# Performance work log

Measured on AMD Instinct MI355X. Metric: run time of the kernel, lower is better.

Reference implementation:

```python
import jax, jax.numpy as jnp
import numpy as np

B, ES, HS, NL, NOUT, T = 16384, 64, 64, 3, 2, 128


def setup_inputs() -> dict:
    key = jax.random.key(0)
    ks = jax.random.split(key, 9)
    k = 1.0 / np.sqrt(HS)
    u = lambda kk, shape: jax.random.uniform(kk, shape, jnp.float32, -k, k)
    return {
        "agentFutureTrajEnc": jax.random.normal(ks[0], (B, ES), jnp.float32),
        "emb_w": u(ks[1], (ES, ES)),
        "emb_b": u(ks[2], (ES,)),
        "w_ih": u(ks[3], (NL, 3 * HS, ES)),
        "w_hh": u(ks[4], (NL, 3 * HS, HS)),
        "b_ih": u(ks[5], (NL, 3 * HS)),
        "b_hh": u(ks[6], (NL, 3 * HS)),
        "out_w": u(ks[7], (NOUT, HS)),
        "out_b": u(ks[8], (NOUT,)),
        "target_length": T,
        "batch_size": B,
    }


def _gru_cell(x, h, Wi, Wh, bi, bh):
    # PyTorch GRU cell math: gates ordered (r, z, n)
    gi = x @ Wi.T + bi            # (B, 3*hs)
    gh = h @ Wh.T + bh            # (B, 3*hs)
    ir, iz, inn = jnp.split(gi, 3, axis=-1)
    hr, hz, hn = jnp.split(gh, 3, axis=-1)
    r = jax.nn.sigmoid(ir + hr)
    z = jax.nn.sigmoid(iz + hz)
    n = jnp.tanh(inn + r * hn)
    return (1.0 - z) * n + z * h


def reference(agentFutureTrajEnc, emb_w, emb_b, w_ih, w_hh, b_ih, b_hh, out_w, out_b,
              target_length, batch_size):
    nl = w_ih.shape[0]
    # hidden initialized by repeating the encoding across layers: (nl, B, hs)
    h0 = jnp.broadcast_to(agentFutureTrajEnc[None], (nl,) + agentFutureTrajEnc.shape)

    def step(carry, _):
        x, h = carry                      # x: (B, es), h: (nl, B, hs)
        inp = x @ emb_w.T + emb_b         # embedding Linear(es->es)
        new_h = []
        for l in range(nl):               # small fixed layer loop
            hl = _gru_cell(inp, h[l], w_ih[l], w_hh[l], b_ih[l], b_hh[l])
            new_h.append(hl)
            inp = hl
        h = jnp.stack(new_h)              # (nl, B, hs)
        out = inp @ out_w.T + out_b       # (B, nout)
        return (h[-1], h), out            # next input is top-layer hidden

    _, outs = jax.lax.scan(step, (agentFutureTrajEnc, h0), None, length=target_length)
    return jnp.transpose(outs, (1, 0, 2))  # (B, T, nout)
```

## Files before the change

### kernel.cpp

```cpp
#include <hip/hip_runtime.h>


#define ESZ   64
#define HSZ   64
#define TLEN  128
#define NOUTC 2
#define NT    2
#define LDW   72
#define TB32  (32*LDW)
#define L2E   1.44269504f

typedef _Float16 half8 __attribute__((ext_vector_type(8)));
typedef _Float16 half4 __attribute__((ext_vector_type(4)));
typedef float    floatx4 __attribute__((ext_vector_type(4)));
typedef float    floatx2 __attribute__((ext_vector_type(2)));

#define MFMA(a, b, c) __builtin_amdgcn_mfma_f32_16x16x32_f16((a), (b), (c), 0, 0, 0)

__global__ __launch_bounds__(768, 3) void gru_pipe(
    const float* __restrict__ enc,
    const float* __restrict__ emb_w,
    const float* __restrict__ emb_b,
    const float* __restrict__ w_ih,
    const float* __restrict__ w_hh,
    const float* __restrict__ b_ih,
    const float* __restrict__ b_hh,
    const float* __restrict__ out_w,
    const float* __restrict__ out_b,
    float* __restrict__ out)
{
    __shared__ _Float16 s_hl[3 * NT * 2 * TB32];
    __shared__ float    s_btmp[3 * 64];
    __shared__ int      s_flag[3 * NT];

    const int tid  = threadIdx.x;
    const int wave = tid >> 6, lane = tid & 63;
    const int l = wave >> 2, g = wave & 3;
    const int q = lane >> 4, c = lane & 15;
    const int u  = (g << 4) | c;
    const int u4 = (g << 4) | (q << 2);
    const long wgbase = (long)blockIdx.x * 64;

    if (tid < 512) {
        const int row = tid >> 3, k0 = (tid & 7) << 3;
        const int j = row >> 5, rr = row & 31;
        const float* p = enc + (wgbase + row) * ESZ + k0;
        floatx4 s0 = *(const floatx4*)p;
        floatx4 s1 = *(const floatx4*)(p + 4);
        half8 v;
        #pragma unroll
        for (int x = 0; x < 4; ++x) { v[x] = (_Float16)s0[x]; v[4 + x] = (_Float16)s1[x]; }
        #pragma unroll
        for (int ly = 0; ly < 3; ++ly)
            *(half8*)&s_hl[((ly * NT + j) * 2 + 1) * TB32 + rr * LDW + k0] = v;
    }
    if (tid < 3 * NT) s_flag[tid] = 0;

    auto ldw8s = [&](const float* p, float sc) {
        floatx4 a = *(const floatx4*)p, b = *(const floatx4*)(p + 4);
        half8 v;
        #pragma unroll
        for (int x = 0; x < 4; ++x) { v[x] = (_Float16)(a[x] * sc); v[4 + x] = (_Float16)(b[x] * sc); }
        return v;
    };
    half8 fR[4], fZ[4], fNi[2], fNh[2], fO[2];
    fO[0] = fO[1] = half8{};
    if (l == 0) {
        const float* wi = w_ih;
        const float* wh = w_hh;
        floatx4 aR[4], aZ[4], aN[4];
        #pragma unroll
        for (int x = 0; x < 4; ++x) { aR[x] = {0,0,0,0}; aZ[x] = {0,0,0,0}; aN[x] = {0,0,0,0}; }
        float bR = 0.f, bZ = 0.f, bN = 0.f;
        for (int k4 = 0; k4 < 64; k4 += 4) {
            floatx4 wr4 = *(const floatx4*)(wi + (u) * 64 + k4);
            floatx4 wz4 = *(const floatx4*)(wi + (64 + u) * 64 + k4);
            floatx4 wn4 = *(const floatx4*)(wi + (128 + u) * 64 + k4);
            floatx4 be4 = *(const floatx4*)(emb_b + k4);
            #pragma unroll
            for (int kk = 0; kk < 4; ++kk) {
                const float* er = emb_w + (k4 + kk) * 64;
                floatx4 e0 = *(const floatx4*)(er + q * 8);
                floatx4 e1 = *(const floatx4*)(er + q * 8 + 4);
                floatx4 e2 = *(const floatx4*)(er + 32 + q * 8);
                floatx4 e3 = *(const floatx4*)(er + 32 + q * 8 + 4);
                const float wr = wr4[kk], wz = wz4[kk], wn = wn4[kk];
                aR[0] += wr * e0; aR[1] += wr * e1; aR[2] += wr * e2; aR[3] += wr * e3;
                aZ[0] += wz * e0; aZ[1] += wz * e1; aZ[2] += wz * e2; aZ[3] += wz * e3;
                aN[0] += wn * e0; aN[1] += wn * e1; aN[2] += wn * e2; aN[3] += wn * e3;
                bR += wr * be4[kk]; bZ += wz * be4[kk]; bN += wn * be4[kk];
            }
        }
        #pragma unroll
        for (int x = 0; x < 4; ++x) {
            fR[0][x] = (_Float16)(-L2E * aR[0][x]);   fR[0][4 + x] = (_Float16)(-L2E * aR[1][x]);
            fR[1][x] = (_Float16)(-L2E * aR[2][x]);   fR[1][4 + x] = (_Float16)(-L2E * aR[3][x]);
            fZ[0][x] = (_Float16)(-L2E * aZ[0][x]);   fZ[0][4 + x] = (_Float16)(-L2E * aZ[1][x]);
            fZ[1][x] = (_Float16)(-L2E * aZ[2][x]);   fZ[1][4 + x] = (_Float16)(-L2E * aZ[3][x]);
            fNi[0][x] = (_Float16)(2*L2E * aN[0][x]); fNi[0][4 + x] = (_Float16)(2*L2E * aN[1][x]);
            fNi[1][x] = (_Float16)(2*L2E * aN[2][x]); fNi[1][4 + x] = (_Float16)(2*L2E * aN[3][x]);
        }
        fR[2]  = ldw8s(wh + (u) * 64 + q * 8, -L2E);        fR[3]  = ldw8s(wh + (u) * 64 + 32 + q * 8, -L2E);
        fZ[2]  = ldw8s(wh + (64 + u) * 64 + q * 8, -L2E);   fZ[3]  = ldw8s(wh + (64 + u) * 64 + 32 + q * 8, -L2E);
        fNh[0] = ldw8s(wh + (128 + u) * 64 + q * 8, 2*L2E); fNh[1] = ldw8s(wh + (128 + u) * 64 + 32 + q * 8, 2*L2E);
        if (q == 0) {
            s_btmp[u] = bR; s_btmp[64 + u] = bZ; s_btmp[128 + u] = bN;
        }
        const int oc = (c < NOUTC) ? c : 0;
        fO[0] = ldw8s(out_w + oc * 64 + q * 8, 1.f);
        fO[1] = ldw8s(out_w + oc * 64 + 32 + q * 8, 1.f);
    } else {
        const float* wi = w_ih + l * 3 * HSZ * ESZ;
        const float* wh = w_hh + l * 3 * HSZ * ESZ;
        fR[0]  = ldw8s(wi + (u) * 64 + q * 8, -L2E);        fR[1]  = ldw8s(wi + (u) * 64 + 32 + q * 8, -L2E);
        fR[2]  = ldw8s(wh + (u) * 64 + q * 8, -L2E);        fR[3]  = ldw8s(wh + (u) * 64 + 32 + q * 8, -L2E);
        fZ[0]  = ldw8s(wi + (64 + u) * 64 + q * 8, -L2E);   fZ[1]  = ldw8s(wi + (64 + u) * 64 + 32 + q * 8, -L2E);
        fZ[2]  = ldw8s(wh + (64 + u) * 64 + q * 8, -L2E);   fZ[3]  = ldw8s(wh + (64 + u) * 64 + 32 + q * 8, -L2E);
        fNi[0] = ldw8s(wi + (128 + u) * 64 + q * 8, 2*L2E); fNi[1] = ldw8s(wi + (128 + u) * 64 + 32 + q * 8, 2*L2E);
        fNh[0] = ldw8s(wh + (128 + u) * 64 + q * 8, 2*L2E); fNh[1] = ldw8s(wh + (128 + u) * 64 + 32 + q * 8, 2*L2E);
    }
    __syncthreads();

    floatx4 bR4, bZ4, bNi4, bNh4;
    if (l == 0) {
        #pragma unroll
        for (int i = 0; i < 4; ++i) {
            bR4[i]  = -L2E * (s_btmp[u4 + i] + b_ih[u4 + i] + b_hh[u4 + i]);
            bZ4[i]  = -L2E * (s_btmp[64 + u4 + i] + b_ih[64 + u4 + i] + b_hh[64 + u4 + i]);
            bNi4[i] = 2.f * L2E * (s_btmp[128 + u4 + i] + b_ih[128 + u4 + i]);
            bNh4[i] = 2.f * L2E * b_hh[128 + u4 + i];
        }
    } else {
        const int b0 = l * 192;
        floatx4 bi0 = *(const floatx4*)(b_ih + b0 + u4),       bh0 = *(const floatx4*)(b_hh + b0 + u4);
        floatx4 bi1 = *(const floatx4*)(b_ih + b0 + 64 + u4),  bh1 = *(const floatx4*)(b_hh + b0 + 64 + u4);
        floatx4 bi2 = *(const floatx4*)(b_ih + b0 + 128 + u4), bh2 = *(const floatx4*)(b_hh + b0 + 128 + u4);
        #pragma unroll
        for (int i = 0; i < 4; ++i) {
            bR4[i]  = -L2E * (bi0[i] + bh0[i]);
            bZ4[i]  = -L2E * (bi1[i] + bh1[i]);
            bNi4[i] = 2.f * L2E * bi2[i];
            bNh4[i] = 2.f * L2E * bh2[i];
        }
    }
    const float ob0 = out_b[0], ob1 = out_b[1];

    floatx4 ca00 = *(const floatx4*)(enc + (wgbase +  0 + c) * 64 + u4);
    floatx4 ca01 = *(const floatx4*)(enc + (wgbase + 16 + c) * 64 + u4);
    floatx4 ca10 = *(const floatx4*)(enc + (wgbase + 32 + c) * 64 + u4);
    floatx4 ca11 = *(const floatx4*)(enc + (wgbase + 48 + c) * 64 + u4);

    const int ar = c * LDW + (q << 3);
    const int fh = l * NT, fx = ((l == 0) ? 2 : (l - 1)) * NT;
    const int myj = g >> 1, mys = g & 1;

    auto iter = [&](const int j, floatx4& cs0, floatx4& cs1, const int t,
                    const int parh, const int parw) {
        { volatile const int* f = &s_flag[fh + j]; const int tg = 4 * t; while (*f < tg) {} }
        asm volatile("" ::: "memory");
        const _Float16* hb = s_hl + ((fh + j) * 2 + parh) * TB32;
        half8 ah00 = *(const half8*)(hb + ar),             ah01 = *(const half8*)(hb + ar + 32);
        half8 ah10 = *(const half8*)(hb + ar + 16 * LDW),  ah11 = *(const half8*)(hb + ar + 16 * LDW + 32);
        floatx4 accr0 = bR4, accz0 = bZ4, accnh0 = bNh4;
        floatx4 accr1 = bR4, accz1 = bZ4, accnh1 = bNh4;
        accr0  = MFMA(fR[2], ah00, accr0);   accr0  = MFMA(fR[3], ah01, accr0);
        accz0  = MFMA(fZ[2], ah00, accz0);   accz0  = MFMA(fZ[3], ah01, accz0);
        accnh0 = MFMA(fNh[0], ah00, accnh0); accnh0 = MFMA(fNh[1], ah01, accnh0);
        accr1  = MFMA(fR[2], ah10, accr1);   accr1  = MFMA(fR[3], ah11, accr1);
        accz1  = MFMA(fZ[2], ah10, accz1);   accz1  = MFMA(fZ[3], ah11, accz1);
        accnh1 = MFMA(fNh[0], ah10, accnh1); accnh1 = MFMA(fNh[1], ah11, accnh1);
        { volatile const int* f = &s_flag[fx + j]; const int tg = (l == 0) ? 4 * t : 4 * t + 4; while (*f < tg) {} }
        asm volatile("" ::: "memory");
        const _Float16* xb = (l == 0) ? s_hl + ((2 * NT + j) * 2 + parh) * TB32
                                      : s_hl + (((l - 1) * NT + j) * 2 + parw) * TB32;
        half8 bx00 = *(const half8*)(xb + ar),             bx01 = *(const half8*)(xb + ar + 32);
        half8 bx10 = *(const half8*)(xb + ar + 16 * LDW),  bx11 = *(const half8*)(xb + ar + 16 * LDW + 32);
        accr0  = MFMA(fR[0], bx00, accr0);   accr0  = MFMA(fR[1], bx01, accr0);
        accz0  = MFMA(fZ[0], bx00, accz0);   accz0  = MFMA(fZ[1], bx01, accz0);
        floatx4 accni0 = bNi4;
        accni0 = MFMA(fNi[0], bx00, accni0); accni0 = MFMA(fNi[1], bx01, accni0);
        accr1  = MFMA(fR[0], bx10, accr1);   accr1  = MFMA(fR[1], bx11, accr1);
        accz1  = MFMA(fZ[0], bx10, accz1);   accz1  = MFMA(fZ[1], bx11, accz1);
        floatx4 accni1 = bNi4;
        accni1 = MFMA(fNi[0], bx10, accni1); accni1 = MFMA(fNi[1], bx11, accni1);
        _Float16* hw = s_hl + ((fh + j) * 2 + parw) * TB32 + c * LDW + u4;
        {
            half4 hv4; floatx4 hnew;
            #pragma unroll
            for (int i = 0; i < 4; ++i) {
                const float r  = __builtin_amdgcn_rcpf(1.f + __builtin_amdgcn_exp2f(accr0[i]));
                const float z  = __builtin_amdgcn_rcpf(1.f + __builtin_amdgcn_exp2f(accz0[i]));
                const float a  = accni0[i] + r * accnh0[i];
                const float n  = 1.f - 2.f * __builtin_amdgcn_rcpf(1.f + __builtin_amdgcn_exp2f(a));
                const float hv = n + z * (cs0[i] - n);
                hnew[i] = hv; hv4[i] = (_Float16)hv;
            }
            *(half4*)hw = hv4;
            cs0 = hnew;
        }
        {
            half4 hv4; floatx4 hnew;
            #pragma unroll
            for (int i = 0; i < 4; ++i) {
                const float r  = __builtin_amdgcn_rcpf(1.f + __builtin_amdgcn_exp2f(accr1[i]));
                const float z  = __builtin_amdgcn_rcpf(1.f + __builtin_amdgcn_exp2f(accz1[i]));
                const float a  = accni1[i] + r * accnh1[i];
                const float n  = 1.f - 2.f * __builtin_amdgcn_rcpf(1.f + __builtin_amdgcn_exp2f(a));
                const float hv = n + z * (cs1[i] - n);
                hnew[i] = hv; hv4[i] = (_Float16)hv;
            }
            *(half4*)(hw + 16 * LDW) = hv4;
            cs1 = hnew;
        }
        asm volatile("s_waitcnt lgkmcnt(0)" ::: "memory");
        if (lane == 0) atomicAdd(&s_flag[fh + j], 1);
        if (l == 0 && myj == j && t >= 1) {
            const half8 ox0 = mys ? bx10 : bx00;
            const half8 ox1 = mys ? bx11 : bx01;
            floatx4 oa = {ob0, ob1, 0.f, 0.f};
            oa = MFMA(fO[0], ox0, oa);
            oa = MFMA(fO[1], ox1, oa);
            if (q == 0) {
                const long row = wgbase + j * 32 + mys * 16 + c;
                *(floatx2*)(out + (row * TLEN + (t - 1)) * NOUTC) = floatx2{oa[0], oa[1]};
            }
        }
    };

    for (int tt = 0; tt < TLEN; tt += 2) {
        iter(0, ca00, ca01, tt,     1, 0);
        iter(1, ca10, ca11, tt,     1, 0);
        iter(0, ca00, ca01, tt + 1, 0, 1);
        iter(1, ca10, ca11, tt + 1, 0, 1);
    }

    if (l == 0) {
        const int j = myj;
        { volatile const int* f = &s_flag[2 * NT + j]; while (*f < 4 * TLEN) {} }
        asm volatile("" ::: "memory");
        const _Float16* xb = s_hl + ((2 * NT + j) * 2 + 1) * TB32 + mys * 16 * LDW;
        half8 bx0 = *(const half8*)(xb + ar), bx1 = *(const half8*)(xb + ar + 32);
        floatx4 oa = {ob0, ob1, 0.f, 0.f};
        oa = MFMA(fO[0], bx0, oa);
        oa = MFMA(fO[1], bx1, oa);
        if (q == 0) {
            const long row = wgbase + j * 32 + mys * 16 + c;
            *(floatx2*)(out + (row * TLEN + 127) * NOUTC) = floatx2{oa[0], oa[1]};
        }
    }
}

extern "C" void kernel_launch(void* const* d_in, const int* in_sizes, int n_in,
                              void* d_out, int out_size, void* d_ws, size_t ws_size,
                              hipStream_t stream) {
    (void)in_sizes; (void)n_in; (void)d_ws; (void)ws_size; (void)out_size;
    const int grid = 16384 / 64;
    gru_pipe<<<grid, 768, 0, stream>>>(
        (const float*)d_in[0],
        (const float*)d_in[1],
        (const float*)d_in[2],
        (const float*)d_in[3],
        (const float*)d_in[4],
        (const float*)d_in[5],
        (const float*)d_in[6],
        (const float*)d_in[7],
        (const float*)d_in[8],
        (float*)d_out);
}
```

Before: 450.3 us.

## Replace spin-flag layer pipeline with barrier-scheduled wavefront over four row tiles

Drops the per-tile LDS flag counters and busy-wait spinning between the three layer wave groups. Splits the 64-row block into four 16-row tiles and runs a fixed staggered schedule where each layer group handles one tile per phase, with __syncthreads between phases. This removes spin polling and atomics, and each visit now works on a single 16-row tile, so MFMA work per visit is halved. In exchange it adds four block-wide barriers per step, and the tight wavefront may leave some groups idle.

```diff
diff --git a/kernel.cpp b/kernel.cpp
--- a/kernel.cpp
+++ b/kernel.cpp
@@ -5,9 +5,8 @@
 #define HSZ   64
 #define TLEN  128
 #define NOUTC 2
-#define NT    2
 #define LDW   72
-#define TB32  (32*LDW)
+#define TB16  (16*LDW)
 #define L2E   1.44269504f
 
 typedef _Float16 half8 __attribute__((ext_vector_type(8)));
@@ -29,9 +28,8 @@
     const float* __restrict__ out_b,
     float* __restrict__ out)
 {
-    __shared__ _Float16 s_hl[3 * NT * 2 * TB32];
+    __shared__ _Float16 s_hl[3 * 4 * 2 * TB16];
     __shared__ float    s_btmp[3 * 64];
-    __shared__ int      s_flag[3 * NT];
 
     const int tid  = threadIdx.x;
     const int wave = tid >> 6, lane = tid & 63;
@@ -43,7 +41,7 @@
 
     if (tid < 512) {
         const int row = tid >> 3, k0 = (tid & 7) << 3;
-        const int j = row >> 5, rr = row & 31;
+        const int j = row >> 4, rr = row & 15;
         const float* p = enc + (wgbase + row) * ESZ + k0;
         floatx4 s0 = *(const floatx4*)p;
         floatx4 s1 = *(const floatx4*)(p + 4);
@@ -52,9 +50,8 @@
         for (int x = 0; x < 4; ++x) { v[x] = (_Float16)s0[x]; v[4 + x] = (_Float16)s1[x]; }
         #pragma unroll
         for (int ly = 0; ly < 3; ++ly)
-            *(half8*)&s_hl[((ly * NT + j) * 2 + 1) * TB32 + rr * LDW + k0] = v;
-    }
-    if (tid < 3 * NT) s_flag[tid] = 0;
+            *(half8*)&s_hl[((ly * 4 + j) * 2 + 1) * TB16 + rr * LDW + k0] = v;
+    }
 
     auto ldw8s = [&](const float* p, float sc) {
         floatx4 a = *(const floatx4*)p, b = *(const floatx4*)(p + 4);
@@ -145,106 +142,81 @@
     }
     const float ob0 = out_b[0], ob1 = out_b[1];
 
-    floatx4 ca00 = *(const floatx4*)(enc + (wgbase +  0 + c) * 64 + u4);
-    floatx4 ca01 = *(const floatx4*)(enc + (wgbase + 16 + c) * 64 + u4);
-    floatx4 ca10 = *(const floatx4*)(enc + (wgbase + 32 + c) * 64 + u4);
-    floatx4 ca11 = *(const floatx4*)(enc + (wgbase + 48 + c) * 64 + u4);
+    floatx4 ca0 = *(const floatx4*)(enc + (wgbase +  0 + c) * 64 + u4);
+    floatx4 ca1 = *(const floatx4*)(enc + (wgbase + 16 + c) * 64 + u4);
+    floatx4 ca2 = *(const floatx4*)(enc + (wgbase + 32 + c) * 64 + u4);
+    floatx4 ca3 = *(const floatx4*)(enc + (wgbase + 48 + c) * 64 + u4);
 
     const int ar = c * LDW + (q << 3);
-    const int fh = l * NT, fx = ((l == 0) ? 2 : (l - 1)) * NT;
-    const int myj = g >> 1, mys = g & 1;
-
-    auto iter = [&](const int j, floatx4& cs0, floatx4& cs1, const int t,
-                    const int parh, const int parw) {
-        { volatile const int* f = &s_flag[fh + j]; const int tg = 4 * t; while (*f < tg) {} }
-        asm volatile("" ::: "memory");
-        const _Float16* hb = s_hl + ((fh + j) * 2 + parh) * TB32;
-        half8 ah00 = *(const half8*)(hb + ar),             ah01 = *(const half8*)(hb + ar + 32);
-        half8 ah10 = *(const half8*)(hb + ar + 16 * LDW),  ah11 = *(const half8*)(hb + ar + 16 * LDW + 32);
-        floatx4 accr0 = bR4, accz0 = bZ4, accnh0 = bNh4;
-        floatx4 accr1 = bR4, accz1 = bZ4, accnh1 = bNh4;
-        accr0  = MFMA(fR[2], ah00, accr0);   accr0  = MFMA(fR[3], ah01, accr0);
-        accz0  = MFMA(fZ[2], ah00, accz0);   accz0  = MFMA(fZ[3], ah01, accz0);
-        accnh0 = MFMA(fNh[0], ah00, accnh0); accnh0 = MFMA(fNh[1], ah01, accnh0);
-        accr1  = MFMA(fR[2], ah10, accr1);   accr1  = MFMA(fR[3], ah11, accr1);
-        accz1  = MFMA(fZ[2], ah10, accz1);   accz1  = MFMA(fZ[3], ah11, accz1);
-        accnh1 = MFMA(fNh[0], ah10, accnh1); accnh1 = MFMA(fNh[1], ah11, accnh1);
-        { volatile const int* f = &s_flag[fx + j]; const int tg = (l == 0) ? 4 * t : 4 * t + 4; while (*f < tg) {} }
-        asm volatile("" ::: "memory");
-        const _Float16* xb = (l == 0) ? s_hl + ((2 * NT + j) * 2 + parh) * TB32
-                                      : s_hl + (((l - 1) * NT + j) * 2 + parw) * TB32;
-        half8 bx00 = *(const half8*)(xb + ar),             bx01 = *(const half8*)(xb + ar + 32);
-        half8 bx10 = *(const half8*)(xb + ar + 16 * LDW),  bx11 = *(const half8*)(xb + ar + 16 * LDW + 32);
-        accr0  = MFMA(fR[0], bx00, accr0);   accr0  = MFMA(fR[1], bx01, accr0);
-        accz0  = MFMA(fZ[0], bx00, accz0);   accz0  = MFMA(fZ[1], bx01, accz0);
-        floatx4 accni0 = bNi4;
-        accni0 = MFMA(fNi[0], bx00, accni0); accni0 = MFMA(fNi[1], bx01, accni0);
-        accr1  = MFMA(fR[0], bx10, accr1);   accr1  = MFMA(fR[1], bx11, accr1);
-        accz1  = MFMA(fZ[0], bx10, accz1);   accz1  = MFMA(fZ[1], bx11, accz1);
-        floatx4 accni1 = bNi4;
-        accni1 = MFMA(fNi[0], bx10, accni1); accni1 = MFMA(fNi[1], bx11, accni1);
-        _Float16* hw = s_hl + ((fh + j) * 2 + parw) * TB32 + c * LDW + u4;
-        {
-            half4 hv4; floatx4 hnew;
-            #pragma unroll
-            for (int i = 0; i < 4; ++i) {
-                const float r  = __builtin_amdgcn_rcpf(1.f + __builtin_amdgcn_exp2f(accr0[i]));
-                const float z  = __builtin_amdgcn_rcpf(1.f + __builtin_amdgcn_exp2f(accz0[i]));
-                const float a  = accni0[i] + r * accnh0[i];
-                const float n  = 1.f - 2.f * __builtin_amdgcn_rcpf(1.f + __builtin_amdgcn_exp2f(a));
-                const float hv = n + z * (cs0[i] - n);
-                hnew[i] = hv; hv4[i] = (_Float16)hv;
-            }
-            *(half4*)hw = hv4;
-            cs0 = hnew;
-        }
-        {
-            half4 hv4; floatx4 hnew;
-            #pragma unroll
-            for (int i = 0; i < 4; ++i) {
-                const float r  = __builtin_amdgcn_rcpf(1.f + __builtin_amdgcn_exp2f(accr1[i]));
-                const float z  = __builtin_amdgcn_rcpf(1.f + __builtin_amdgcn_exp2f(accz1[i]));
-                const float a  = accni1[i] + r * accnh1[i];
-                const float n  = 1.f - 2.f * __builtin_amdgcn_rcpf(1.f + __builtin_amdgcn_exp2f(a));
-                const float hv = n + z * (cs1[i] - n);
-                hnew[i] = hv; hv4[i] = (_Float16)hv;
-            }
-            *(half4*)(hw + 16 * LDW) = hv4;
-            cs1 = hnew;
-        }
-        asm volatile("s_waitcnt lgkmcnt(0)" ::: "memory");
-        if (lane == 0) atomicAdd(&s_flag[fh + j], 1);
-        if (l == 0 && myj == j && t >= 1) {
-            const half8 ox0 = mys ? bx10 : bx00;
-            const half8 ox1 = mys ? bx11 : bx01;
+
+    auto visit = [&](const int ll, const int j, floatx4& cs, const int t) {
+        const int parw = t & 1;
+        const _Float16* hb = s_hl + ((ll * 4 + j) * 2 + (parw ^ 1)) * TB16;
+        half8 ah0 = *(const half8*)(hb + ar);
+        half8 ah1 = *(const half8*)(hb + ar + 32);
+        floatx4 accr = bR4, accz = bZ4, accnh = bNh4;
+        accr  = MFMA(fR[2], ah0, accr);   accr  = MFMA(fR[3], ah1, accr);
+        accz  = MFMA(fZ[2], ah0, accz);   accz  = MFMA(fZ[3], ah1, accz);
+        accnh = MFMA(fNh[0], ah0, accnh); accnh = MFMA(fNh[1], ah1, accnh);
+        const _Float16* xb = (ll == 0) ? s_hl + ((8 + j) * 2 + (parw ^ 1)) * TB16
+                                       : s_hl + (((ll - 1) * 4 + j) * 2 + parw) * TB16;
+        half8 bx0 = *(const half8*)(xb + ar);
+        half8 bx1 = *(const half8*)(xb + ar + 32);
+        accr = MFMA(fR[0], bx0, accr); accr = MFMA(fR[1], bx1, accr);
+        accz = MFMA(fZ[0], bx0, accz); accz = MFMA(fZ[1], bx1, accz);
+        floatx4 accni = bNi4;
+        accni = MFMA(fNi[0], bx0, accni); accni = MFMA(fNi[1], bx1, accni);
+        _Float16* hw = s_hl + ((ll * 4 + j) * 2 + parw) * TB16 + c * LDW + u4;
+        half4 hv4; floatx4 hnew;
+        #pragma unroll
+        for (int i = 0; i < 4; ++i) {
+            const float r  = __builtin_amdgcn_rcpf(1.f + __builtin_amdgcn_exp2f(accr[i]));
+            const float z  = __builtin_amdgcn_rcpf(1.f + __builtin_amdgcn_exp2f(accz[i]));
+            const float a  = accni[i] + r * accnh[i];
+            const float n  = 1.f - 2.f * __builtin_amdgcn_rcpf(1.f + __builtin_amdgcn_exp2f(a));
+            const float hv = n + z * (cs[i] - n);
+            hnew[i] = hv; hv4[i] = (_Float16)hv;
+        }
+        *(half4*)hw = hv4;
+        cs = hnew;
+        if (ll == 0 && g == j && t >= 1) {
             floatx4 oa = {ob0, ob1, 0.f, 0.f};
-            oa = MFMA(fO[0], ox0, oa);
-            oa = MFMA(fO[1], ox1, oa);
+            oa = MFMA(fO[0], bx0, oa);
+            oa = MFMA(fO[1], bx1, oa);
             if (q == 0) {
-                const long row = wgbase + j * 32 + mys * 16 + c;
+                const long row = wgbase + j * 16 + c;
                 *(floatx2*)(out + (row * TLEN + (t - 1)) * NOUTC) = floatx2{oa[0], oa[1]};
             }
         }
     };
 
-    for (int tt = 0; tt < TLEN; tt += 2) {
-        iter(0, ca00, ca01, tt,     1, 0);
-        iter(1, ca10, ca11, tt,     1, 0);
-        iter(0, ca00, ca01, tt + 1, 0, 1);
-        iter(1, ca10, ca11, tt + 1, 0, 1);
+    for (int s4 = 0; s4 < 129; ++s4) {
+        if (l == 0)      { if (s4 < TLEN) visit(0, 0, ca0, s4); }
+        else if (l == 1) { if (s4 >= 1)   visit(1, 3, ca3, s4 - 1); }
+        else             { if (s4 >= 1)   visit(2, 2, ca2, s4 - 1); }
+        __syncthreads();
+        if (l == 0)      { if (s4 < TLEN) visit(0, 1, ca1, s4); }
+        else if (l == 1) { if (s4 < TLEN) visit(1, 0, ca0, s4); }
+        else             { if (s4 >= 1)   visit(2, 3, ca3, s4 - 1); }
+        __syncthreads();
+        if (l == 0)      { if (s4 < TLEN) visit(0, 2, ca2, s4); }
+        else if (l == 1) { if (s4 < TLEN) visit(1, 1, ca1, s4); }
+        else             { if (s4 < TLEN) visit(2, 0, ca0, s4); }
+        __syncthreads();
+        if (l == 0)      { if (s4 < TLEN) visit(0, 3, ca3, s4); }
+        else if (l == 1) { if (s4 < TLEN) visit(1, 2, ca2, s4); }
+        else             { if (s4 < TLEN) visit(2, 1, ca1, s4); }
+        __syncthreads();
     }
 
     if (l == 0) {
-        const int j = myj;
-        { volatile const int* f = &s_flag[2 * NT + j]; while (*f < 4 * TLEN) {} }
-        asm volatile("" ::: "memory");
-        const _Float16* xb = s_hl + ((2 * NT + j) * 2 + 1) * TB32 + mys * 16 * LDW;
+        const _Float16* xb = s_hl + ((8 + g) * 2 + 1) * TB16;
         half8 bx0 = *(const half8*)(xb + ar), bx1 = *(const half8*)(xb + ar + 32);
         floatx4 oa = {ob0, ob1, 0.f, 0.f};
         oa = MFMA(fO[0], bx0, oa);
         oa = MFMA(fO[1], bx1, oa);
         if (q == 0) {
-            const long row = wgbase + j * 32 + mys * 16 + c;
+            const long row = wgbase + g * 16 + c;
             *(floatx2*)(out + (row * TLEN + 127) * NOUTC) = floatx2{oa[0], oa[1]};
         }
     }
```

Measured after the change: 459.4 us. +2.0%, slower.
